# Optimization experiments

Hardware: AMD Instinct MI355X
Metric: run time of the kernel (lower is better)

The kernel has to match this reference:

```python
import jax, jax.numpy as jnp
import numpy as np
import math

N_LAYERS = 8
D = 1024
H = 16
DK = D // H
T = 1024
V = 32000
B = 2
DFF = 4 * D
EPS = 1e-5


def layernorm(x, scale, bias):
    mu = jnp.mean(x, axis=-1, keepdims=True)
    var = jnp.mean(jnp.square(x - mu), axis=-1, keepdims=True)
    return (x - mu) * jax.lax.rsqrt(var + EPS) * scale + bias


def setup_inputs() -> dict:
    key = jax.random.key(0)
    ks = jax.random.split(key, 32)
    s = 0.02
    rn = lambda k, shape: jax.random.normal(k, shape, dtype=jnp.float32) * s
    x = jax.random.randint(ks[0], (B, T), 0, V)
    return {
        "x": x,
        "inp_emb": rn(ks[1], (V, D)),
        "pos_emb": rn(ks[2], (T, D)),
        # per-layer weights stacked on leading layer axis; per-head wq/wk/wv are
        # concatenated along the output dim (mathematically identical to the
        # per-head nn.Linear list in the torch code)
        "wq": rn(ks[3], (N_LAYERS, D, D)), "bq": jnp.zeros((N_LAYERS, D), jnp.float32),
        "wk": rn(ks[4], (N_LAYERS, D, D)), "bk": jnp.zeros((N_LAYERS, D), jnp.float32),
        "wv": rn(ks[5], (N_LAYERS, D, D)), "bv": jnp.zeros((N_LAYERS, D), jnp.float32),
        "wo": rn(ks[6], (N_LAYERS, D, D)), "bo": jnp.zeros((N_LAYERS, D), jnp.float32),
        "w1": rn(ks[7], (N_LAYERS, D, DFF)), "b1": jnp.zeros((N_LAYERS, DFF), jnp.float32),
        "w2": rn(ks[8], (N_LAYERS, DFF, D)), "b2": jnp.zeros((N_LAYERS, D), jnp.float32),
        "ln1_s": jnp.ones((N_LAYERS, D), jnp.float32), "ln1_b": jnp.zeros((N_LAYERS, D), jnp.float32),
        "ln2_s": jnp.ones((N_LAYERS, D), jnp.float32), "ln2_b": jnp.zeros((N_LAYERS, D), jnp.float32),
        "lno_s": jnp.ones((D,), jnp.float32), "lno_b": jnp.zeros((D,), jnp.float32),
        "w_out": rn(ks[9], (D, V)),
    }


def reference(x, inp_emb, pos_emb, wq, bq, wk, bk, wv, bv, wo, bo,
              w1, b1, w2, b2, ln1_s, ln1_b, ln2_s, ln2_b, lno_s, lno_b, w_out):
    h = inp_emb[x] + pos_emb[jnp.arange(T)]            # [B,T,D]
    causal = jnp.tril(jnp.ones((T, T), dtype=bool))    # [T,T]
    scale = 1.0 / math.sqrt(DK)
    for i in range(N_LAYERS):
        # --- multi-head causal attention ---
        xn = layernorm(h, ln1_s[i], ln1_b[i])
        q = (xn @ wq[i] + bq[i]).reshape(B, T, H, DK)
        k = (xn @ wk[i] + bk[i]).reshape(B, T, H, DK)
        v = (xn @ wv[i] + bv[i]).reshape(B, T, H, DK)
        scores = jnp.einsum('bqhd,bkhd->bhqk', q, k) * scale
        scores = jnp.where(causal, scores, -jnp.inf)
        att = jax.nn.softmax(scores, axis=-1)           # [B,H,T,T]
        y = jnp.einsum('bhqk,bkhd->bqhd', att, v).reshape(B, T, D)
        h = h + y @ wo[i] + bo[i]
        # --- feed-forward ---
        xn = layernorm(h, ln2_s[i], ln2_b[i])
        h = h + jax.nn.gelu(xn @ w1[i] + b1[i], approximate=False) @ w2[i] + b2[i]
    h = layernorm(h, lno_s, lno_b)
    return h @ w_out                                    # logits [B,T,V]
```

## Files before the change

### kernel.cpp

```cpp
#include <hip/hip_runtime.h>
#include <cmath>

#define D_MODEL 1024
#define N_HEADS 16
#define DKH     64
#define SEQ_T   1024
#define BATCH   2
#define VOCAB   32000
#define DFF_    4096
#define NLAYERS 8

typedef __bf16 bf16x8 __attribute__((ext_vector_type(8)));
typedef __bf16 bf16x4v __attribute__((ext_vector_type(4)));
typedef float  f32x4  __attribute__((ext_vector_type(4)));

__device__ __forceinline__ float gelu_f(float x) {
    return 0.5f * x * (1.0f + erff(x * 0.70710678118654752f));
}

__device__ __forceinline__ void gload_lds16(const void* g, void* l) {
    __builtin_amdgcn_global_load_lds(
        (const __attribute__((address_space(1))) void*)g,
        (__attribute__((address_space(3))) void*)l, 16, 0, 0);
}

__global__ __launch_bounds__(256) void embed_kernel(
    const int* __restrict__ x, const float* __restrict__ inp_emb,
    const float* __restrict__ pos_emb, float* __restrict__ h)
{
    const int idx = blockIdx.x * 256 + threadIdx.x;
    const int bt  = idx >> 10;
    const int d   = idx & 1023;
    const int t   = bt & (SEQ_T - 1);
    const int tok = x[bt];
    h[idx] = inp_emb[(size_t)tok * D_MODEL + d] + pos_emb[(size_t)t * D_MODEL + d];
}

__global__ __launch_bounds__(256) void layernorm_kernel(
    const float* __restrict__ x, const float* __restrict__ sc,
    const float* __restrict__ bi, __bf16* __restrict__ o)
{
    const int row = blockIdx.x;
    const int tid = threadIdx.x;
    const int c   = tid * 4;
    const float4 v = *(const float4*)(x + (size_t)row * D_MODEL + c);
    float sum = v.x + v.y + v.z + v.w;
    float sq  = v.x * v.x + v.y * v.y + v.z * v.z + v.w * v.w;
    #pragma unroll
    for (int off = 32; off > 0; off >>= 1) {
        sum += __shfl_xor(sum, off);
        sq  += __shfl_xor(sq, off);
    }
    __shared__ float ssum[4], ssq[4];
    const int wave = tid >> 6, lane = tid & 63;
    if (lane == 0) { ssum[wave] = sum; ssq[wave] = sq; }
    __syncthreads();
    sum = ssum[0] + ssum[1] + ssum[2] + ssum[3];
    sq  = ssq[0]  + ssq[1]  + ssq[2]  + ssq[3];
    const float mu  = sum * (1.0f / D_MODEL);
    const float var = sq * (1.0f / D_MODEL) - mu * mu;
    const float rs  = rsqrtf(var + 1e-5f);
    const float4 s4 = *(const float4*)(sc + c);
    const float4 b4 = *(const float4*)(bi + c);
    bf16x4v ov;
    ov[0] = (__bf16)((v.x - mu) * rs * s4.x + b4.x);
    ov[1] = (__bf16)((v.y - mu) * rs * s4.y + b4.y);
    ov[2] = (__bf16)((v.z - mu) * rs * s4.z + b4.z);
    ov[3] = (__bf16)((v.w - mu) * rs * s4.w + b4.w);
    *(bf16x4v*)(o + (size_t)row * D_MODEL + c) = ov;
}

__global__ __launch_bounds__(256) void prep_layer_kernel(
    const float* __restrict__ wq, const float* __restrict__ wk,
    const float* __restrict__ wv, const float* __restrict__ wo,
    const float* __restrict__ w1, const float* __restrict__ w2,
    const float* __restrict__ bq, const float* __restrict__ bk,
    const float* __restrict__ bv,
    __bf16* __restrict__ wqkvT, __bf16* __restrict__ woT,
    __bf16* __restrict__ w1T, __bf16* __restrict__ w2T,
    float* __restrict__ bqkv)
{
    __shared__ __bf16 tile[32][36];
    const int b   = blockIdx.x;
    const int tid = threadIdx.x;

    if (b >= 12288) {
        const int j = (b - 12288) * 256 + tid;
        bqkv[j] = (j < 1024) ? bq[j] : (j < 2048 ? bk[j - 1024] : bv[j - 2048]);
        return;
    }

    const float* in;
    __bf16* out;
    int K, N, kb0, nb0;
    if (b < 4096) {
        const int w = b >> 10, t = b & 1023;
        K = 1024; N = 1024; kb0 = (t >> 5) * 32; nb0 = (t & 31) * 32;
        in  = (w == 0) ? wq : (w == 1) ? wk : (w == 2) ? wv : wo;
        out = (w == 3) ? woT : wqkvT + (size_t)w * 1024 * 1024;
    } else if (b < 8192) {
        const int t = b - 4096;
        K = 1024; N = 4096; kb0 = (t >> 7) * 32; nb0 = (t & 127) * 32;
        in = w1; out = w1T;
    } else {
        const int t = b - 8192;
        K = 4096; N = 1024; kb0 = (t >> 5) * 32; nb0 = (t & 31) * 32;
        in = w2; out = w2T;
    }

    {
        const int rr = tid >> 3, c4 = (tid & 7) * 4;
        const float4 v = *(const float4*)(in + (size_t)(kb0 + rr) * N + nb0 + c4);
        tile[rr][c4 + 0] = (__bf16)v.x;
        tile[rr][c4 + 1] = (__bf16)v.y;
        tile[rr][c4 + 2] = (__bf16)v.z;
        tile[rr][c4 + 3] = (__bf16)v.w;
    }
    __syncthreads();
    {
        const int cc = tid >> 3, r4 = (tid & 7) * 4;
        bf16x4v ov;
        ov[0] = tile[r4 + 0][cc];
        ov[1] = tile[r4 + 1][cc];
        ov[2] = tile[r4 + 2][cc];
        ov[3] = tile[r4 + 3][cc];
        *(bf16x4v*)(out + (size_t)(nb0 + cc) * K + kb0 + r4) = ov;
    }
}

__global__ __launch_bounds__(256) void wout_tr_kernel(
    const float* __restrict__ in, __bf16* __restrict__ out)
{
    __shared__ __bf16 tile[32][36];
    const int tid = threadIdx.x;
    const int nb0 = (blockIdx.x >> 5) * 32;
    const int kb0 = (blockIdx.x & 31) * 32;
    {
        const int rr = tid >> 3, c4 = (tid & 7) * 4;
        const float4 v = *(const float4*)(in + (size_t)(kb0 + rr) * VOCAB + nb0 + c4);
        tile[rr][c4 + 0] = (__bf16)v.x;
        tile[rr][c4 + 1] = (__bf16)v.y;
        tile[rr][c4 + 2] = (__bf16)v.z;
        tile[rr][c4 + 3] = (__bf16)v.w;
    }
    __syncthreads();
    {
        const int cc = tid >> 3, r4 = (tid & 7) * 4;
        bf16x4v ov;
        ov[0] = tile[r4 + 0][cc];
        ov[1] = tile[r4 + 1][cc];
        ov[2] = tile[r4 + 2][cc];
        ov[3] = tile[r4 + 3][cc];
        *(bf16x4v*)(out + (size_t)(nb0 + cc) * D_MODEL + kb0 + r4) = ov;
    }
}

template <int BN_T, int EPI, typename OutT>
__global__ __launch_bounds__(256) void gemm_bt(
    const __bf16* __restrict__ A, const __bf16* __restrict__ Bt,
    const float* __restrict__ bias, const float* __restrict__ res,
    OutT* __restrict__ C, int M, int N, int K)
{
    constexpr int NF  = BN_T / 32;
    constexpr int NCB = BN_T / 8;
    __shared__ __bf16 As[2][128 * 64];
    __shared__ __bf16 Bs[2][BN_T * 64];

    const int tid  = threadIdx.x;
    const int wave = tid >> 6;
    const int lane = tid & 63;
    const int r    = lane & 15;
    const int kb   = lane >> 4;
    const int wm   = wave >> 1;
    const int wn   = wave & 1;

    const int ntm = gridDim.x;
    const int nwg = ntm * gridDim.y;
    int bid = blockIdx.y * ntm + blockIdx.x;
    if ((nwg & 7) == 0) bid = (bid & 7) * (nwg >> 3) + (bid >> 3);
    const int bm = (bid % ntm) * 128;
    const int bn = (bid / ntm) * BN_T;

    const int srow = lane >> 3;
    const int sg   = lane & 7;

    f32x4 acc[4][NF] = {};

    auto stage = [&](int buf, int k0) {
        #pragma unroll
        for (int i = 0; i < 4; ++i) {
            const int c    = i * 4 + wave;
            const int row  = c * 8 + srow;
            const int scol = (sg ^ (row & 7)) * 8;
            gload_lds16(A + (size_t)(bm + row) * K + k0 + scol, &As[buf][c * 512]);
        }
        #pragma unroll
        for (int i = 0; i < NCB / 4; ++i) {
            const int c    = i * 4 + wave;
            const int row  = c * 8 + srow;
            const int scol = (sg ^ (row & 7)) * 8;
            gload_lds16(Bt + (size_t)(bn + row) * K + k0 + scol, &Bs[buf][c * 512]);
        }
    };

    stage(0, 0);
    __syncthreads();

    int cur = 0;
    for (int k0 = 0; k0 < K; k0 += 64) {
        if (k0 + 64 < K) stage(cur ^ 1, k0 + 64);
        #pragma unroll
        for (int s = 0; s < 2; ++s) {
            bf16x8 af[4];
            #pragma unroll
            for (int m = 0; m < 4; ++m) {
                const int row = wm * 64 + m * 16 + r;
                const int g   = (s * 4 + kb) ^ (row & 7);
                af[m] = *(const bf16x8*)&As[cur][row * 64 + g * 8];
            }
            #pragma unroll
            for (int n = 0; n < NF; ++n) {
                const int row = wn * (NF * 16) + n * 16 + r;
                const int g   = (s * 4 + kb) ^ (row & 7);
                const bf16x8 bfr = *(const bf16x8*)&Bs[cur][row * 64 + g * 8];
                #pragma unroll
                for (int m = 0; m < 4; ++m)
                    acc[m][n] = __builtin_amdgcn_mfma_f32_16x16x32_bf16(af[m], bfr, acc[m][n], 0, 0, 0);
            }
        }
        __syncthreads();
        cur ^= 1;
    }

    #pragma unroll
    for (int m = 0; m < 4; ++m) {
        const int row = bm + wm * 64 + m * 16 + kb * 4;
        #pragma unroll
        for (int n = 0; n < NF; ++n) {
            const int col = bn + wn * (NF * 16) + n * 16 + r;
            const float bv = bias ? bias[col] : 0.0f;
            #pragma unroll
            for (int rg = 0; rg < 4; ++rg) {
                float v = acc[m][n][rg] + bv;
                if constexpr (EPI == 1) v += res[(size_t)(row + rg) * N + col];
                if constexpr (EPI == 2) v = gelu_f(v);
                C[(size_t)(row + rg) * N + col] = (OutT)v;
            }
        }
    }
}

__global__ __launch_bounds__(256) void attn_mfma_kernel(
    const __bf16* __restrict__ qkv, __bf16* __restrict__ y)
{
    constexpr int QS = 3 * D_MODEL;
    __shared__ __align__(16) __bf16 K_lds[64][72];
    __shared__ __align__(16) __bf16 V_lds[64][72];
    __shared__ __align__(16) __bf16 P_lds[4][16][72];

    const int tid  = threadIdx.x;
    const int wave = tid >> 6;
    const int lane = tid & 63;
    const int r    = lane & 15;
    const int kb   = lane >> 4;

    const int q0 = blockIdx.x * 64;
    const int b  = blockIdx.y >> 4;
    const int h  = blockIdx.y & 15;

    const __bf16* qp = qkv + (size_t)b * SEQ_T * QS + h * DKH;
    const __bf16* kp = qp + D_MODEL;
    const __bf16* vp = qp + 2 * D_MODEL;
    __bf16* yp = y + (size_t)b * SEQ_T * D_MODEL + h * DKH;

    bf16x8 qf[2];
    {
        const int qrow = q0 + wave * 16 + r;
        #pragma unroll
        for (int kc = 0; kc < 2; ++kc)
            qf[kc] = *(const bf16x8*)(qp + (size_t)qrow * QS + kc * 32 + kb * 8);
    }

    float m_run[4] = {-INFINITY, -INFINITY, -INFINITY, -INFINITY};
    float l_run[4] = {0.0f, 0.0f, 0.0f, 0.0f};
    f32x4 yacc[4] = {};

    const int skey = tid >> 2;
    const int sg   = (tid & 3) * 16;

    const int ntiles = blockIdx.x + 1;
    for (int kt = 0; kt < ntiles; ++kt) {
        {
            const size_t go = (size_t)(kt * 64 + skey) * QS;
            *(bf16x8*)&K_lds[skey][sg]     = *(const bf16x8*)(kp + go + sg);
            *(bf16x8*)&K_lds[skey][sg + 8] = *(const bf16x8*)(kp + go + sg + 8);
            const bf16x8 v0 = *(const bf16x8*)(vp + go + sg);
            const bf16x8 v1 = *(const bf16x8*)(vp + go + sg + 8);
            #pragma unroll
            for (int j = 0; j < 8; ++j) V_lds[sg + j][skey]     = v0[j];
            #pragma unroll
            for (int j = 0; j < 8; ++j) V_lds[sg + 8 + j][skey] = v1[j];
        }
        __syncthreads();

        f32x4 sacc[4] = {};
        #pragma unroll
        for (int kc = 0; kc < 2; ++kc) {
            #pragma unroll
            for (int g = 0; g < 4; ++g) {
                const bf16x8 kf = *(const bf16x8*)&K_lds[g * 16 + r][kc * 32 + kb * 8];
                sacc[g] = __builtin_amdgcn_mfma_f32_16x16x32_bf16(qf[kc], kf, sacc[g], 0, 0, 0);
            }
        }

        float s[4][4], p[4][4];
        #pragma unroll
        for (int g = 0; g < 4; ++g) {
            const int key = kt * 64 + g * 16 + r;
            #pragma unroll
            for (int rg = 0; rg < 4; ++rg) {
                const int qq = q0 + wave * 16 + kb * 4 + rg;
                s[g][rg] = (key <= qq) ? sacc[g][rg] * 0.125f : -INFINITY;
            }
        }
        float mt[4], mn[4], corr[4], psum[4];
        #pragma unroll
        for (int rg = 0; rg < 4; ++rg)
            mt[rg] = fmaxf(fmaxf(s[0][rg], s[1][rg]), fmaxf(s[2][rg], s[3][rg]));
        #pragma unroll
        for (int off = 1; off < 16; off <<= 1) {
            #pragma unroll
            for (int rg = 0; rg < 4; ++rg) mt[rg] = fmaxf(mt[rg], __shfl_xor(mt[rg], off));
        }
        #pragma unroll
        for (int rg = 0; rg < 4; ++rg) {
            mn[rg]  = fmaxf(m_run[rg], mt[rg]);
            psum[rg] = 0.0f;
            #pragma unroll
            for (int g = 0; g < 4; ++g) {
                p[g][rg] = __expf(s[g][rg] - mn[rg]);
                psum[rg] += p[g][rg];
            }
        }
        #pragma unroll
        for (int off = 1; off < 16; off <<= 1) {
            #pragma unroll
            for (int rg = 0; rg < 4; ++rg) psum[rg] += __shfl_xor(psum[rg], off);
        }
        #pragma unroll
        for (int rg = 0; rg < 4; ++rg) {
            corr[rg] = __expf(m_run[rg] - mn[rg]);
            l_run[rg] = l_run[rg] * corr[rg] + psum[rg];
            m_run[rg] = mn[rg];
        }
        #pragma unroll
        for (int n = 0; n < 4; ++n) {
            #pragma unroll
            for (int rg = 0; rg < 4; ++rg) yacc[n][rg] *= corr[rg];
        }

        #pragma unroll
        for (int g = 0; g < 4; ++g) {
            #pragma unroll
            for (int rg = 0; rg < 4; ++rg)
                P_lds[wave][kb * 4 + rg][g * 16 + r] = (__bf16)p[g][rg];
        }
        const bf16x8 pa0 = *(const bf16x8*)&P_lds[wave][r][kb * 8];
        const bf16x8 pa1 = *(const bf16x8*)&P_lds[wave][r][32 + kb * 8];

        #pragma unroll
        for (int n = 0; n < 4; ++n) {
            const bf16x8 vf0 = *(const bf16x8*)&V_lds[n * 16 + r][kb * 8];
            yacc[n] = __builtin_amdgcn_mfma_f32_16x16x32_bf16(pa0, vf0, yacc[n], 0, 0, 0);
        }
        #pragma unroll
        for (int n = 0; n < 4; ++n) {
            const bf16x8 vf1 = *(const bf16x8*)&V_lds[n * 16 + r][32 + kb * 8];
            yacc[n] = __builtin_amdgcn_mfma_f32_16x16x32_bf16(pa1, vf1, yacc[n], 0, 0, 0);
        }
        __syncthreads();
    }

    float inv[4];
    #pragma unroll
    for (int rg = 0; rg < 4; ++rg) inv[rg] = 1.0f / l_run[rg];
    #pragma unroll
    for (int n = 0; n < 4; ++n) {
        #pragma unroll
        for (int rg = 0; rg < 4; ++rg) {
            const int row = q0 + wave * 16 + kb * 4 + rg;
            yp[(size_t)row * D_MODEL + n * 16 + r] = (__bf16)(yacc[n][rg] * inv[rg]);
        }
    }
}

extern "C" void kernel_launch(void* const* d_in, const int* in_sizes, int n_in,
                              void* d_out, int out_size, void* d_ws, size_t ws_size,
                              hipStream_t stream)
{
    const int*   x       = (const int*)  d_in[0];
    const float* inp_emb = (const float*)d_in[1];
    const float* pos_emb = (const float*)d_in[2];
    const float* wq = (const float*)d_in[3];
    const float* bq = (const float*)d_in[4];
    const float* wk = (const float*)d_in[5];
    const float* bk = (const float*)d_in[6];
    const float* wv = (const float*)d_in[7];
    const float* bv = (const float*)d_in[8];
    const float* wo = (const float*)d_in[9];
    const float* bo = (const float*)d_in[10];
    const float* w1 = (const float*)d_in[11];
    const float* b1 = (const float*)d_in[12];
    const float* w2 = (const float*)d_in[13];
    const float* b2 = (const float*)d_in[14];
    const float* ln1_s = (const float*)d_in[15];
    const float* ln1_b = (const float*)d_in[16];
    const float* ln2_s = (const float*)d_in[17];
    const float* ln2_b = (const float*)d_in[18];
    const float* lno_s = (const float*)d_in[19];
    const float* lno_b = (const float*)d_in[20];
    const float* w_out = (const float*)d_in[21];

    const int M = BATCH * SEQ_T;
    const size_t MB = 1u << 20;

    char* w = (char*)d_ws;
    float*  h     = (float*) (w + 0);
    __bf16* xn    = (__bf16*)(w + 8  * MB);
    __bf16* yb    = (__bf16*)(w + 12 * MB);
    __bf16* sh    = (__bf16*)(w + 16 * MB);
    __bf16* wqkvT = (__bf16*)(w + 32 * MB);
    __bf16* woT   = (__bf16*)(w + 38 * MB);
    __bf16* w1T   = (__bf16*)(w + 40 * MB);
    __bf16* w2T   = (__bf16*)(w + 48 * MB);
    float*  bqkv  = (float*) (w + 56 * MB);
    __bf16* woutT = (__bf16*)(w + 57 * MB);

    embed_kernel<<<dim3(M * D_MODEL / 256), 256, 0, stream>>>(x, inp_emb, pos_emb, h);

    for (int i = 0; i < NLAYERS; ++i) {
        const size_t wOff  = (size_t)i * D_MODEL * D_MODEL;
        const size_t w1Off = (size_t)i * D_MODEL * DFF_;

        prep_layer_kernel<<<dim3(12300), 256, 0, stream>>>(
            wq + wOff, wk + wOff, wv + wOff, wo + wOff, w1 + w1Off, w2 + w1Off,
            bq + i * D_MODEL, bk + i * D_MODEL, bv + i * D_MODEL,
            wqkvT, woT, w1T, w2T, bqkv);

        layernorm_kernel<<<dim3(M), 256, 0, stream>>>(h, ln1_s + i * D_MODEL, ln1_b + i * D_MODEL, xn);
        gemm_bt<128, 0, __bf16><<<dim3(M / 128, 3 * D_MODEL / 128), 256, 0, stream>>>(
            xn, wqkvT, bqkv, nullptr, sh, M, 3 * D_MODEL, D_MODEL);
        attn_mfma_kernel<<<dim3(SEQ_T / 64, BATCH * N_HEADS), 256, 0, stream>>>(sh, yb);
        gemm_bt<64, 1, float><<<dim3(M / 128, D_MODEL / 64), 256, 0, stream>>>(
            yb, woT, bo + i * D_MODEL, h, h, M, D_MODEL, D_MODEL);
        layernorm_kernel<<<dim3(M), 256, 0, stream>>>(h, ln2_s + i * D_MODEL, ln2_b + i * D_MODEL, xn);
        gemm_bt<128, 2, __bf16><<<dim3(M / 128, DFF_ / 128), 256, 0, stream>>>(
            xn, w1T, b1 + i * DFF_, nullptr, sh, M, DFF_, D_MODEL);
        gemm_bt<64, 1, float><<<dim3(M / 128, D_MODEL / 64), 256, 0, stream>>>(
            sh, w2T, b2 + i * D_MODEL, h, h, M, D_MODEL, DFF_);
    }

    wout_tr_kernel<<<dim3((VOCAB / 32) * 32), 256, 0, stream>>>(w_out, woutT);
    layernorm_kernel<<<dim3(M), 256, 0, stream>>>(h, lno_s, lno_b, xn);
    gemm_bt<128, 0, float><<<dim3(M / 128, VOCAB / 128), 256, 0, stream>>>(
        xn, woutT, nullptr, nullptr, (float*)d_out, M, VOCAB, D_MODEL);
}
```

Measured before the change: 1.830 ms.

## Widen attention blocks, swizzle V in LDS, single-buffer GEMM, nontemporal logits

The attention kernel now runs 512 threads over 128 query rows per block, so each loaded K/V tile serves twice as many queries. K/V staging uses one 16-byte chunk per thread, and V's transposed LDS layout is XOR-swizzled to cut bank conflicts. The GEMM drops LDS double buffering for a single buffer with a sync before compute, which halves LDS use and may allow more resident blocks but gives up load/compute overlap. The final vocab GEMM writes logits with nontemporal stores to avoid polluting cache.

Result: no change. 1.831 ms (+0.0%).

```diff
diff --git a/kernel.cpp b/kernel.cpp
--- a/kernel.cpp
+++ b/kernel.cpp
@@ -155,7 +155,7 @@
     }
 }
 
-template <int BN_T, int EPI, typename OutT>
+template <int BN_T, int EPI, typename OutT, bool NT = false>
 __global__ __launch_bounds__(256) void gemm_bt(
     const __bf16* __restrict__ A, const __bf16* __restrict__ Bt,
     const float* __restrict__ bias, const float* __restrict__ res,
@@ -163,8 +163,8 @@
 {
     constexpr int NF  = BN_T / 32;
     constexpr int NCB = BN_T / 8;
-    __shared__ __bf16 As[2][128 * 64];
-    __shared__ __bf16 Bs[2][BN_T * 64];
+    __shared__ __bf16 As[128 * 64];
+    __shared__ __bf16 Bs[BN_T * 64];
 
     const int tid  = threadIdx.x;
     const int wave = tid >> 6;
@@ -186,29 +186,23 @@
 
     f32x4 acc[4][NF] = {};
 
-    auto stage = [&](int buf, int k0) {
+    for (int k0 = 0; k0 < K; k0 += 64) {
         #pragma unroll
         for (int i = 0; i < 4; ++i) {
             const int c    = i * 4 + wave;
             const int row  = c * 8 + srow;
             const int scol = (sg ^ (row & 7)) * 8;
-            gload_lds16(A + (size_t)(bm + row) * K + k0 + scol, &As[buf][c * 512]);
+            gload_lds16(A + (size_t)(bm + row) * K + k0 + scol, &As[c * 512]);
         }
         #pragma unroll
         for (int i = 0; i < NCB / 4; ++i) {
             const int c    = i * 4 + wave;
             const int row  = c * 8 + srow;
             const int scol = (sg ^ (row & 7)) * 8;
-            gload_lds16(Bt + (size_t)(bn + row) * K + k0 + scol, &Bs[buf][c * 512]);
-        }
-    };
-
-    stage(0, 0);
-    __syncthreads();
-
-    int cur = 0;
-    for (int k0 = 0; k0 < K; k0 += 64) {
-        if (k0 + 64 < K) stage(cur ^ 1, k0 + 64);
+            gload_lds16(Bt + (size_t)(bn + row) * K + k0 + scol, &Bs[c * 512]);
+        }
+        __syncthreads();
+
         #pragma unroll
         for (int s = 0; s < 2; ++s) {
             bf16x8 af[4];
@@ -216,20 +210,19 @@
             for (int m = 0; m < 4; ++m) {
                 const int row = wm * 64 + m * 16 + r;
                 const int g   = (s * 4 + kb) ^ (row & 7);
-                af[m] = *(const bf16x8*)&As[cur][row * 64 + g * 8];
+                af[m] = *(const bf16x8*)&As[row * 64 + g * 8];
             }
             #pragma unroll
             for (int n = 0; n < NF; ++n) {
                 const int row = wn * (NF * 16) + n * 16 + r;
                 const int g   = (s * 4 + kb) ^ (row & 7);
-                const bf16x8 bfr = *(const bf16x8*)&Bs[cur][row * 64 + g * 8];
+                const bf16x8 bfr = *(const bf16x8*)&Bs[row * 64 + g * 8];
                 #pragma unroll
                 for (int m = 0; m < 4; ++m)
                     acc[m][n] = __builtin_amdgcn_mfma_f32_16x16x32_bf16(af[m], bfr, acc[m][n], 0, 0, 0);
             }
         }
         __syncthreads();
-        cur ^= 1;
     }
 
     #pragma unroll
@@ -244,19 +237,23 @@
                 float v = acc[m][n][rg] + bv;
                 if constexpr (EPI == 1) v += res[(size_t)(row + rg) * N + col];
                 if constexpr (EPI == 2) v = gelu_f(v);
-                C[(size_t)(row + rg) * N + col] = (OutT)v;
-            }
-        }
-    }
-}
-
-__global__ __launch_bounds__(256) void attn_mfma_kernel(
+                if constexpr (NT) {
+                    __builtin_nontemporal_store((OutT)v, &C[(size_t)(row + rg) * N + col]);
+                } else {
+                    C[(size_t)(row + rg) * N + col] = (OutT)v;
+                }
+            }
+        }
+    }
+}
+
+__global__ __launch_bounds__(512) void attn_mfma_kernel(
     const __bf16* __restrict__ qkv, __bf16* __restrict__ y)
 {
     constexpr int QS = 3 * D_MODEL;
     __shared__ __align__(16) __bf16 K_lds[64][72];
     __shared__ __align__(16) __bf16 V_lds[64][72];
-    __shared__ __align__(16) __bf16 P_lds[4][16][72];
+    __shared__ __align__(16) __bf16 P_lds[8][16][72];
 
     const int tid  = threadIdx.x;
     const int wave = tid >> 6;
@@ -264,7 +261,7 @@
     const int r    = lane & 15;
     const int kb   = lane >> 4;
 
-    const int q0 = blockIdx.x * 64;
+    const int q0 = blockIdx.x * 128;
     const int b  = blockIdx.y >> 4;
     const int h  = blockIdx.y & 15;
 
@@ -285,21 +282,19 @@
     float l_run[4] = {0.0f, 0.0f, 0.0f, 0.0f};
     f32x4 yacc[4] = {};
 
-    const int skey = tid >> 2;
-    const int sg   = (tid & 3) * 16;
-
-    const int ntiles = blockIdx.x + 1;
+    const int skey = tid >> 3;
+    const int sg8  = (tid & 7) * 8;
+
+    const int ntiles = (q0 >> 6) + 2;
     for (int kt = 0; kt < ntiles; ++kt) {
         {
             const size_t go = (size_t)(kt * 64 + skey) * QS;
-            *(bf16x8*)&K_lds[skey][sg]     = *(const bf16x8*)(kp + go + sg);
-            *(bf16x8*)&K_lds[skey][sg + 8] = *(const bf16x8*)(kp + go + sg + 8);
-            const bf16x8 v0 = *(const bf16x8*)(vp + go + sg);
-            const bf16x8 v1 = *(const bf16x8*)(vp + go + sg + 8);
-            #pragma unroll
-            for (int j = 0; j < 8; ++j) V_lds[sg + j][skey]     = v0[j];
-            #pragma unroll
-            for (int j = 0; j < 8; ++j) V_lds[sg + 8 + j][skey] = v1[j];
+            *(bf16x8*)&K_lds[skey][sg8] = *(const bf16x8*)(kp + go + sg8);
+            const bf16x8 vv = *(const bf16x8*)(vp + go + sg8);
+            const int swz = (sg8 >> 3) * 8;
+            #pragma unroll
+            for (int j = 0; j < 8; ++j)
+                V_lds[sg8 + j][skey ^ swz] = vv[j];
         }
         __syncthreads();
 
@@ -370,12 +365,16 @@
 
         #pragma unroll
         for (int n = 0; n < 4; ++n) {
-            const bf16x8 vf0 = *(const bf16x8*)&V_lds[n * 16 + r][kb * 8];
+            const int vrow = n * 16 + r;
+            const int swz  = (vrow >> 3) & 7;
+            const bf16x8 vf0 = *(const bf16x8*)&V_lds[vrow][(kb ^ swz) * 8];
             yacc[n] = __builtin_amdgcn_mfma_f32_16x16x32_bf16(pa0, vf0, yacc[n], 0, 0, 0);
         }
         #pragma unroll
         for (int n = 0; n < 4; ++n) {
-            const bf16x8 vf1 = *(const bf16x8*)&V_lds[n * 16 + r][32 + kb * 8];
+            const int vrow = n * 16 + r;
+            const int swz  = (vrow >> 3) & 7;
+            const bf16x8 vf1 = *(const bf16x8*)&V_lds[vrow][((kb + 4) ^ swz) * 8];
             yacc[n] = __builtin_amdgcn_mfma_f32_16x16x32_bf16(pa1, vf1, yacc[n], 0, 0, 0);
         }
         __syncthreads();
@@ -450,7 +449,7 @@
         layernorm_kernel<<<dim3(M), 256, 0, stream>>>(h, ln1_s + i * D_MODEL, ln1_b + i * D_MODEL, xn);
         gemm_bt<128, 0, __bf16><<<dim3(M / 128, 3 * D_MODEL / 128), 256, 0, stream>>>(
             xn, wqkvT, bqkv, nullptr, sh, M, 3 * D_MODEL, D_MODEL);
-        attn_mfma_kernel<<<dim3(SEQ_T / 64, BATCH * N_HEADS), 256, 0, stream>>>(sh, yb);
+        attn_mfma_kernel<<<dim3(SEQ_T / 128, BATCH * N_HEADS), 512, 0, stream>>>(sh, yb);
         gemm_bt<64, 1, float><<<dim3(M / 128, D_MODEL / 64), 256, 0, stream>>>(
             yb, woT, bo + i * D_MODEL, h, h, M, D_MODEL, D_MODEL);
         layernorm_kernel<<<dim3(M), 256, 0, stream>>>(h, ln2_s + i * D_MODEL, ln2_b + i * D_MODEL, xn);
@@ -462,6 +461,6 @@
 
     wout_tr_kernel<<<dim3((VOCAB / 32) * 32), 256, 0, stream>>>(w_out, woutT);
     layernorm_kernel<<<dim3(M), 256, 0, stream>>>(h, lno_s, lno_b, xn);
-    gemm_bt<128, 0, float><<<dim3(M / 128, VOCAB / 128), 256, 0, stream>>>(
+    gemm_bt<128, 0, float, true><<<dim3(M / 128, VOCAB / 128), 256, 0, stream>>>(
         xn, woutT, nullptr, nullptr, (float*)d_out, M, VOCAB, D_MODEL);
 }
```
